# Performance work log

Hardware: AMD Instinct MI355X
Metric: run time of the kernel (lower is better)

## Reference

```python
import jax, jax.numpy as jnp
import numpy as np
import math

D = 2048
H = 8
DK = D // H // 2  # 128
NL = 3
EPS = 1e-6
SCALE = 1.0 / math.sqrt(DK)


def _ln(x, g, b):
    m = jnp.mean(x, axis=-1, keepdims=True)
    v = jnp.mean(jnp.square(x - m), axis=-1, keepdims=True)
    return (x - m) * jax.lax.rsqrt(v + EPS) * g + b


def _attn_layer(x, g, b, Wq, Wk, Wv):
    bs = x.shape[0]
    xn = _ln(x, g, b)
    # torch Linear: y = x @ W.T ; reshape to (bs, h, 2, d_k)
    q = (xn @ Wq.T).reshape(bs, H, 2, DK)
    k = (xn @ Wk.T).reshape(bs, H, 2, DK)
    v = (xn @ Wv.T).reshape(bs, H, 2, DK)
    s = jnp.einsum('bhpd,bhqd->bhpq', q, k) * SCALE  # tiny 2x2 scores
    a = jax.nn.softmax(s, axis=-1)
    o = jnp.einsum('bhpq,bhqd->bhpd', a, v).reshape(bs, D)
    return o + x


def _ff_layer(x, lnd_g, lnd_b, lnt_g, lnt_b, Wd1, bd1, Wd2, bd2, Wt1, bt1, Wt2, bt2):
    d, t = x[:, :D // 2], x[:, D // 2:]
    dn = _ln(d, lnd_g, lnd_b)
    tn = _ln(t, lnt_g, lnt_b)
    do = jax.nn.relu(dn @ Wd1.T + bd1) @ Wd2.T + bd2
    to = jax.nn.relu(tn @ Wt1.T + bt1) @ Wt2.T + bt2
    return jnp.concatenate([do, to], axis=-1) + x


def setup_inputs() -> dict:
    key = jax.random.key(0)
    ks = iter(jax.random.split(key, 64))
    s = 0.02
    inp = {}
    inp['x'] = jax.random.normal(next(ks), (8192, D), dtype=jnp.float32)
    # attention stacks: NL layers
    inp['attn_ln_g'] = jnp.ones((NL, D), jnp.float32)
    inp['attn_ln_b'] = jnp.zeros((NL, D), jnp.float32)
    inp['Wq'] = jax.random.normal(next(ks), (NL, D, D), jnp.float32) * s
    inp['Wk'] = jax.random.normal(next(ks), (NL, D, D), jnp.float32) * s
    inp['Wv'] = jax.random.normal(next(ks), (NL, D, D), jnp.float32) * s
    # feedforward stacks: NL-1 layers
    F = NL - 1
    hd = D // 2
    inp['ff_lnd_g'] = jnp.ones((F, hd), jnp.float32)
    inp['ff_lnd_b'] = jnp.zeros((F, hd), jnp.float32)
    inp['ff_lnt_g'] = jnp.ones((F, hd), jnp.float32)
    inp['ff_lnt_b'] = jnp.zeros((F, hd), jnp.float32)
    inp['Wd1'] = jax.random.normal(next(ks), (F, D, hd), jnp.float32) * s
    inp['bd1'] = jnp.zeros((F, D), jnp.float32)
    inp['Wd2'] = jax.random.normal(next(ks), (F, hd, D), jnp.float32) * s
    inp['bd2'] = jnp.zeros((F, hd), jnp.float32)
    inp['Wt1'] = jax.random.normal(next(ks), (F, D, hd), jnp.float32) * s
    inp['bt1'] = jnp.zeros((F, D), jnp.float32)
    inp['Wt2'] = jax.random.normal(next(ks), (F, hd, D), jnp.float32) * s
    inp['bt2'] = jnp.zeros((F, hd), jnp.float32)
    # output head
    inp['Wo1'] = jax.random.normal(next(ks), (hd, D), jnp.float32) * s
    inp['bo1'] = jnp.zeros((hd,), jnp.float32)
    inp['Wo2'] = jax.random.normal(next(ks), (1, hd), jnp.float32) * s
    inp['bo2'] = jnp.zeros((1,), jnp.float32)
    return inp


def reference(x, attn_ln_g, attn_ln_b, Wq, Wk, Wv,
              ff_lnd_g, ff_lnd_b, ff_lnt_g, ff_lnt_b,
              Wd1, bd1, Wd2, bd2, Wt1, bt1, Wt2, bt2,
              Wo1, bo1, Wo2, bo2):
    for n in range(NL - 1):
        x = _attn_layer(x, attn_ln_g[n], attn_ln_b[n], Wq[n], Wk[n], Wv[n])
        x = _ff_layer(x, ff_lnd_g[n], ff_lnd_b[n], ff_lnt_g[n], ff_lnt_b[n],
                      Wd1[n], bd1[n], Wd2[n], bd2[n], Wt1[n], bt1[n], Wt2[n], bt2[n])
    x = _attn_layer(x, attn_ln_g[-1], attn_ln_b[-1], Wq[-1], Wk[-1], Wv[-1])
    h = jax.nn.relu(x @ Wo1.T + bo1)
    return h @ Wo2.T + bo2  # [bs, 1]
```

## Files before the change

### kernel.cpp

```cpp
#include <hip/hip_runtime.h>
#include <stdint.h>


typedef __bf16 bf16x8 __attribute__((ext_vector_type(8)));
typedef float f32x4 __attribute__((ext_vector_type(4)));

static __device__ __forceinline__ float bf2f(unsigned short u) {
  unsigned int x = ((unsigned int)u) << 16;
  float f;
  __builtin_memcpy(&f, &x, 4);
  return f;
}
static __device__ __forceinline__ unsigned short f2bf(float f) {
  unsigned int x;
  __builtin_memcpy(&x, &f, 4);
  x += 0x7fffu + ((x >> 16) & 1u);
  return (unsigned short)(x >> 16);
}

static __device__ __forceinline__ void gload_lds16(const void* g, void* l) {
  __builtin_amdgcn_global_load_lds(
      (const __attribute__((address_space(1))) unsigned int*)g,
      (__attribute__((address_space(3))) unsigned int*)l, 16, 0, 0);
}

__global__ __launch_bounds__(256) void cvt_kernel(
    const float* __restrict__ in, unsigned short* __restrict__ out, long n) {
  const long i = ((long)blockIdx.x * 256 + threadIdx.x) * 4;
  if (i + 3 < n) {
    float4 f = *(const float4*)(in + i);
    *(ushort4*)(out + i) = make_ushort4(f2bf(f.x), f2bf(f.y), f2bf(f.z), f2bf(f.w));
  }
}

#define MAXSEG 14
struct CvtArgs {
  const float* src[MAXSEG];
  unsigned short* dst[MAXSEG];
  long pfx[MAXSEG + 1];
  int ns;
};
__global__ __launch_bounds__(256) void cvt_multi_kernel(CvtArgs a) {
  const long i = ((long)blockIdx.x * 256 + threadIdx.x) * 4;
  int s = 0;
  while (s + 1 < a.ns && i >= a.pfx[s + 1]) ++s;
  const long off = i - a.pfx[s];
  float4 f = *(const float4*)(a.src[s] + off);
  *(ushort4*)(a.dst[s] + off) =
      make_ushort4(f2bf(f.x), f2bf(f.y), f2bf(f.z), f2bf(f.w));
}

#define BARRIER __builtin_amdgcn_s_barrier()
#define LGKM(N)                                                     \
  do {                                                              \
    asm volatile("s_waitcnt lgkmcnt(" #N ")" ::: "memory");         \
    __builtin_amdgcn_sched_barrier(0);                              \
  } while (0)
#define VMC(N)                                                      \
  do {                                                              \
    asm volatile("s_waitcnt vmcnt(" #N ")" ::: "memory");           \
    __builtin_amdgcn_sched_barrier(0);                              \
  } while (0)

__global__ __launch_bounds__(512, 2) void gemm8_kernel(
    const unsigned short* __restrict__ A, int lda,
    const unsigned short* __restrict__ B, int K,
    void* __restrict__ Cp, int ldc, const float* __restrict__ bias,
    int relu, int out_f32, int resadd,
    const unsigned short* __restrict__ A2, const unsigned short* __restrict__ B2,
    void* __restrict__ C2p, const float* __restrict__ bias2, int dual) {
  extern __shared__ __align__(16) char smem[];

  const int tid = threadIdx.x;
  const int lane = tid & 63;
  const int w = tid >> 6;
  const int wm = w >> 2;
  const int wn = w & 3;

  const int gx = (int)gridDim.x;
  const int nwg = gx * (int)gridDim.y;
  const int orig = (int)blockIdx.y * gx + (int)blockIdx.x;
  const int qch = nwg >> 3, rch = nwg & 7, xcd = orig & 7, io = orig >> 3;
  const int wgid =
      (xcd < rch ? xcd * (qch + 1) : rch * (qch + 1) + (xcd - rch) * qch) + io;
  const int bx = wgid % gx;
  const int by = wgid / gx;
  const long brow = (long)by * 256;

  const unsigned short* Ap = A;
  const unsigned short* Bp = B;
  const float* bi = bias;
  void* Cq = Cp;
  long bcol;
  if (dual && bx >= (gx >> 1)) {
    Ap = A2; Bp = B2; bi = bias2; Cq = C2p;
    bcol = (long)(bx - (gx >> 1)) * 256;
  } else {
    bcol = (long)bx * 256;
  }

  const int NT = K >> 6;

  const int lrA = tid >> 3;
  const int scb = ((tid & 7) * 16) ^ (((tid >> 3) & 7) << 4);
  const unsigned wb = (unsigned)(tid & ~63) * 16;
  const long ldab = (long)lda * 2;
  const long ldbb = (long)K * 2;
  const char* gA = (const char*)Ap + (brow + lrA) * ldab + scb;
  const char* gB = (const char*)Bp + (bcol + lrA) * ldbb + scb;
  const long a64 = 64 * ldab, a128 = 128 * ldab, a192 = 192 * ldab;
  const long b64 = 64 * ldbb, b128 = 128 * ldbb, b192 = 192 * ldbb;

#define STAGE_A(bb, off)                                        \
  do {                                                          \
    gload_lds16(gA + (off), smem + (bb) + wb);                  \
    gload_lds16(gA + a64 + (off), smem + (bb) + 8192 + wb);     \
    gload_lds16(gA + a128 + (off), smem + (bb) + 16384 + wb);   \
    gload_lds16(gA + a192 + (off), smem + (bb) + 24576 + wb);   \
  } while (0)
#define STAGE_B(bb, off)                                        \
  do {                                                          \
    gload_lds16(gB + (off), smem + (bb) + 32768 + wb);          \
    gload_lds16(gB + b64 + (off), smem + (bb) + 40960 + wb);    \
    gload_lds16(gB + b128 + (off), smem + (bb) + 49152 + wb);   \
    gload_lds16(gB + b192 + (off), smem + (bb) + 57344 + wb);   \
  } while (0)

  f32x4 acc[8][4];
  const f32x4 fz = {0.f, 0.f, 0.f, 0.f};
#pragma unroll
  for (int m = 0; m < 8; ++m)
#pragma unroll
    for (int n = 0; n < 4; ++n) acc[m][n] = fz;

  const int frow = lane & 15;
  const int fkb = (lane >> 4) * 16;
  const int fswz = (lane & 7) << 4;

#define RDA(dst, CB, M, KK)                                                   \
  dst = *(const bf16x8*)(smem + (CB) + (wm * 128 + (M) * 16 + frow) * 128 +   \
                         (((KK) * 64 + fkb) ^ fswz))
#define RDB(dst, CB, N, KK)                                                   \
  dst = *(const bf16x8*)(smem + (CB) + 32768 +                                \
                         (wn * 64 + (N) * 16 + frow) * 128 +                  \
                         (((KK) * 64 + fkb) ^ fswz))

#define MM8(AF, MA, BF, NA, MO, NO)                                           \
  do {                                                                        \
    _Pragma("unroll") for (int kk = 0; kk < 2; ++kk)                          \
    _Pragma("unroll") for (int mm = 0; mm < 2; ++mm)                          \
    _Pragma("unroll") for (int nn = 0; nn < 2; ++nn)                          \
        acc[(MO) + mm][(NO) + nn] = __builtin_amdgcn_mfma_f32_16x16x32_bf16(  \
            AF[(MA) + mm][kk], BF[(NA) + nn][kk], acc[(MO) + mm][(NO) + nn],  \
            0, 0, 0);                                                         \
  } while (0)
#define MM8N(AF, BF, NB, NO)                                                  \
  do {                                                                        \
    _Pragma("unroll") for (int kk = 0; kk < 2; ++kk)                          \
    _Pragma("unroll") for (int mm = 0; mm < 4; ++mm)                          \
        acc[mm][(NO)] = __builtin_amdgcn_mfma_f32_16x16x32_bf16(              \
            AF[mm][kk], BF[(NB)][kk], acc[mm][(NO)], 0, 0, 0);                \
  } while (0)

  bf16x8 afL[4][2], afH[4][2], bfvL[2][2], bfvH[2][2];

  STAGE_A(0, 0);
  STAGE_B(0, 0);
  STAGE_A(65536, 128);
  STAGE_B(65536, 128);
  VMC(8);
  BARRIER;
  long soff = 256;

#define TILE_IT(T, CB)                                                        \
  do {                                                                        \
                            \
    RDB(bfvL[0][0], CB, 0, 0); RDB(bfvL[0][1], CB, 0, 1);                     \
    RDB(bfvL[1][0], CB, 1, 0); RDB(bfvL[1][1], CB, 1, 1);                     \
    RDA(afL[0][0], CB, 0, 0); RDA(afL[0][1], CB, 0, 1);                       \
    RDA(afL[1][0], CB, 1, 0); RDA(afL[1][1], CB, 1, 1);                       \
    RDA(afL[2][0], CB, 2, 0); RDA(afL[2][1], CB, 2, 1);                       \
    RDA(afL[3][0], CB, 3, 0); RDA(afL[3][1], CB, 3, 1);                       \
    LGKM(8);                    \
    BARRIER;                                                                  \
    LGKM(0);                                                                  \
    __builtin_amdgcn_s_setprio(1);                                            \
    MM8(afL, 0, bfvL, 0, 0, 0);                                               \
    MM8(afL, 2, bfvL, 0, 2, 0);                                               \
    __builtin_amdgcn_s_setprio(0);                                            \
    BARRIER;                                                                  \
                                              \
    RDB(bfvH[0][0], CB, 2, 0); RDB(bfvH[0][1], CB, 2, 1);                     \
    RDB(bfvH[1][0], CB, 3, 0); RDB(bfvH[1][1], CB, 3, 1);                     \
    BARRIER;                                                                  \
    LGKM(0);                                                                  \
    __builtin_amdgcn_s_setprio(1);                                            \
    MM8N(afL, bfvH, 0, 2);                                                    \
    MM8N(afL, bfvH, 1, 3);                                                    \
    __builtin_amdgcn_s_setprio(0);                                            \
    BARRIER;                                                                  \
                 \
                                \
    RDA(afH[0][0], CB, 4, 0); RDA(afH[0][1], CB, 4, 1);                       \
    RDA(afH[1][0], CB, 5, 0); RDA(afH[1][1], CB, 5, 1);                       \
    RDA(afH[2][0], CB, 6, 0); RDA(afH[2][1], CB, 6, 1);                       \
    RDA(afH[3][0], CB, 7, 0); RDA(afH[3][1], CB, 7, 1);                       \
    if ((T) + 2 < NT) STAGE_B(CB, soff);                                      \
    BARRIER;                                                                  \
    LGKM(0);                                                                  \
    __builtin_amdgcn_s_setprio(1);                                            \
    MM8(afH, 0, bfvL, 0, 4, 0);                                               \
    MM8(afH, 2, bfvL, 0, 6, 0);                                               \
    __builtin_amdgcn_s_setprio(0);                                            \
    BARRIER;                                                                  \
                 \
                                \
    if ((T) + 2 < NT) {                                                       \
      STAGE_A(CB, soff);                                                      \
      VMC(8);                                      \
    } else {                                                                  \
      VMC(0);                                                 \
    }                                                                         \
    BARRIER;                                                                  \
    __builtin_amdgcn_s_setprio(1);                                            \
    MM8(afH, 0, bfvH, 0, 4, 2);                                               \
    MM8(afH, 2, bfvH, 0, 6, 2);                                               \
    __builtin_amdgcn_s_setprio(0);                                            \
    BARRIER;                                                                  \
    soff += 128;                                                              \
  } while (0)

  for (int t = 0; t < NT; t += 2) {
    TILE_IT(t, 0);
    TILE_IT(t + 1, 65536);
  }

  const long rb0 = brow + wm * 128 + (lane >> 4) * 4;
  const long cb0 = bcol + wn * 64 + (lane & 15);
#pragma unroll
  for (int m = 0; m < 8; ++m) {
#pragma unroll
    for (int n = 0; n < 4; ++n) {
      const long col = cb0 + n * 16;
      const float bv = bi ? bi[col] : 0.f;
#pragma unroll
      for (int j = 0; j < 4; ++j) {
        const long r = rb0 + m * 16 + j;
        float v = acc[m][n][j] + bv;
        if (relu) v = fmaxf(v, 0.f);
        if (out_f32) {
          float* cp = (float*)Cq + r * (long)ldc + col;
          if (resadd) v += *cp;
          *cp = v;
        } else {
          ((unsigned short*)Cq)[r * (long)ldc + col] = f2bf(v);
        }
      }
    }
  }
#undef TILE_IT
#undef STAGE_A
#undef STAGE_B
#undef RDA
#undef RDB
#undef MM8
#undef MM8N
}

__global__ __launch_bounds__(256) void gemm_bt_kernel(
    const unsigned short* __restrict__ A, int lda,
    const unsigned short* __restrict__ B, int K,
    void* __restrict__ Cp, int ldc,
    const float* __restrict__ bias,
    const void* __restrict__ res, int res_mode, int ldres,
    int relu, int out_f32) {
  __shared__ __align__(16) unsigned short As[128 * 32];
  __shared__ __align__(16) unsigned short Bs[128 * 32];

  const int t = threadIdx.x;
  const int lane = t & 63;
  const int w = t >> 6;
  const int wr = (w >> 1) * 64;
  const int wc = (w & 1) * 64;
  const long brow = (long)blockIdx.y * 128;
  const long bcol = (long)blockIdx.x * 128;

  const int srow = lane >> 2;
  const int scol = (lane & 3) * 8;
  const unsigned short* Ab = A + (brow + w * 32 + srow) * (long)lda + scol;
  const unsigned short* Bb = B + (bcol + w * 32 + srow) * (long)K + scol;
  unsigned short* Asb = &As[(w * 32) * 32];
  unsigned short* Bsb = &Bs[(w * 32) * 32];

  f32x4 acc[4][4];
  const f32x4 fzero = {0.f, 0.f, 0.f, 0.f};
#pragma unroll
  for (int m = 0; m < 4; ++m)
#pragma unroll
    for (int n = 0; n < 4; ++n) acc[m][n] = fzero;

  const int fr = lane & 15;
  const int fk = (lane >> 4) * 8;

  for (int kt = 0; kt < K; kt += 32) {
    gload_lds16(Ab + kt, Asb);
    gload_lds16(Ab + 16 * (long)lda + kt, Asb + 16 * 32);
    gload_lds16(Bb + kt, Bsb);
    gload_lds16(Bb + 16 * (long)K + kt, Bsb + 16 * 32);
    __syncthreads();

    bf16x8 af[4], bfv[4];
#pragma unroll
    for (int m = 0; m < 4; ++m)
      af[m] = *(const bf16x8*)&As[(wr + m * 16 + fr) * 32 + fk];
#pragma unroll
    for (int n = 0; n < 4; ++n)
      bfv[n] = *(const bf16x8*)&Bs[(wc + n * 16 + fr) * 32 + fk];
#pragma unroll
    for (int m = 0; m < 4; ++m)
#pragma unroll
      for (int n = 0; n < 4; ++n)
        acc[m][n] = __builtin_amdgcn_mfma_f32_16x16x32_bf16(af[m], bfv[n],
                                                            acc[m][n], 0, 0, 0);
    __syncthreads();
  }

  const long rbase = brow + wr + (lane >> 4) * 4;
#pragma unroll
  for (int m = 0; m < 4; ++m) {
#pragma unroll
    for (int n = 0; n < 4; ++n) {
      const long col = bcol + wc + n * 16 + fr;
      const float bv = bias ? bias[col] : 0.f;
#pragma unroll
      for (int j = 0; j < 4; ++j) {
        const long r = rbase + m * 16 + j;
        float v = acc[m][n][j] + bv;
        if (relu) v = fmaxf(v, 0.f);
        if (res_mode == 1)
          v += ((const float*)res)[r * (long)ldres + col];
        else if (res_mode == 2)
          v += bf2f(((const unsigned short*)res)[r * (long)ldres + col]);
        if (out_f32)
          ((float*)Cp)[r * (long)ldc + col] = v;
        else
          ((unsigned short*)Cp)[r * (long)ldc + col] = f2bf(v);
      }
    }
  }
}

template <int L>
__global__ __launch_bounds__(256) void ln_kernel(
    const void* __restrict__ inp, int in_bf16, int ldin,
    const float* __restrict__ g, const float* __restrict__ b,
    unsigned short* __restrict__ outp, int ldout) {
  constexpr int VEC = L / 256;
  const long row = blockIdx.x;
  const int t = threadIdx.x;
  float v[VEC];
  if (in_bf16) {
    const unsigned short* p = (const unsigned short*)inp + row * (long)ldin + t * VEC;
#pragma unroll
    for (int i = 0; i < VEC; i += 4) {
      ushort4 u = *(const ushort4*)(p + i);
      v[i] = bf2f(u.x); v[i + 1] = bf2f(u.y); v[i + 2] = bf2f(u.z); v[i + 3] = bf2f(u.w);
    }
  } else {
    const float* p = (const float*)inp + row * (long)ldin + t * VEC;
#pragma unroll
    for (int i = 0; i < VEC; i += 4) {
      float4 f = *(const float4*)(p + i);
      v[i] = f.x; v[i + 1] = f.y; v[i + 2] = f.z; v[i + 3] = f.w;
    }
  }
  float s = 0.f, sq = 0.f;
#pragma unroll
  for (int i = 0; i < VEC; ++i) { s += v[i]; sq += v[i] * v[i]; }
#pragma unroll
  for (int off = 32; off; off >>= 1) {
    s += __shfl_xor(s, off, 64);
    sq += __shfl_xor(sq, off, 64);
  }
  __shared__ float red[8];
  if ((t & 63) == 0) { red[t >> 6] = s; red[4 + (t >> 6)] = sq; }
  __syncthreads();
  s = red[0] + red[1] + red[2] + red[3];
  sq = red[4] + red[5] + red[6] + red[7];
  const float mean = s * (1.f / L);
  const float var = sq * (1.f / L) - mean * mean;
  const float rstd = rsqrtf(var + 1e-6f);
  unsigned short* op = outp + row * (long)ldout + t * VEC;
  const float* gp = g + t * VEC;
  const float* bp = b + t * VEC;
#pragma unroll
  for (int i = 0; i < VEC; i += 4) {
    float4 gg = *(const float4*)(gp + i);
    float4 bb = *(const float4*)(bp + i);
    *(ushort4*)(op + i) = make_ushort4(
        f2bf((v[i + 0] - mean) * rstd * gg.x + bb.x),
        f2bf((v[i + 1] - mean) * rstd * gg.y + bb.y),
        f2bf((v[i + 2] - mean) * rstd * gg.z + bb.z),
        f2bf((v[i + 3] - mean) * rstd * gg.w + bb.w));
  }
}

__global__ __launch_bounds__(512) void attn_glue_kernel(
    const unsigned short* __restrict__ Q, const unsigned short* __restrict__ Kq,
    const unsigned short* __restrict__ V, int ld, const void* __restrict__ Xres,
    int res_bf16, void* __restrict__ Xout, int out_bf16,
    unsigned short* __restrict__ Xout_bf,
    unsigned short* __restrict__ DNp, unsigned short* __restrict__ TNp,
    const float* __restrict__ lnd_g, const float* __restrict__ lnd_b,
    const float* __restrict__ lnt_g, const float* __restrict__ lnt_b) {
  const long row = blockIdx.x;
  const int h = threadIdx.x >> 6;
  const int lane = threadIdx.x & 63;
  const long qbase = row * (long)ld + h * 256;
  const long xbase = row * 2048 + h * 256;
  const int d = lane * 2;

  ushort2 q0 = *(const ushort2*)&Q[qbase + d];
  ushort2 q1 = *(const ushort2*)&Q[qbase + 128 + d];
  ushort2 k0 = *(const ushort2*)&Kq[qbase + d];
  ushort2 k1 = *(const ushort2*)&Kq[qbase + 128 + d];
  ushort2 v0 = *(const ushort2*)&V[qbase + d];
  ushort2 v1 = *(const ushort2*)&V[qbase + 128 + d];

  const float q0x = bf2f(q0.x), q0y = bf2f(q0.y);
  const float q1x = bf2f(q1.x), q1y = bf2f(q1.y);
  const float k0x = bf2f(k0.x), k0y = bf2f(k0.y);
  const float k1x = bf2f(k1.x), k1y = bf2f(k1.y);

  float s00 = q0x * k0x + q0y * k0y;
  float s01 = q0x * k1x + q0y * k1y;
  float s10 = q1x * k0x + q1y * k0y;
  float s11 = q1x * k1x + q1y * k1y;
#pragma unroll
  for (int off = 32; off; off >>= 1) {
    s00 += __shfl_xor(s00, off, 64);
    s01 += __shfl_xor(s01, off, 64);
    s10 += __shfl_xor(s10, off, 64);
    s11 += __shfl_xor(s11, off, 64);
  }
  const float SC = 0.088388347648318447f;
  s00 *= SC; s01 *= SC; s10 *= SC; s11 *= SC;
  const float m0 = fmaxf(s00, s01), m1 = fmaxf(s10, s11);
  const float e00 = __expf(s00 - m0), e01 = __expf(s01 - m0);
  const float e10 = __expf(s10 - m1), e11 = __expf(s11 - m1);
  const float i0 = 1.f / (e00 + e01), i1 = 1.f / (e10 + e11);
  const float a00 = e00 * i0, a01 = e01 * i0;
  const float a10 = e10 * i1, a11 = e11 * i1;

  const float v0x = bf2f(v0.x), v0y = bf2f(v0.y);
  const float v1x = bf2f(v1.x), v1y = bf2f(v1.y);
  float o0x = a00 * v0x + a01 * v1x, o0y = a00 * v0y + a01 * v1y;
  float o1x = a10 * v0x + a11 * v1x, o1y = a10 * v0y + a11 * v1y;

  if (res_bf16) {
    const unsigned short* xr = (const unsigned short*)Xres + xbase;
    ushort2 ra = *(const ushort2*)&xr[d];
    ushort2 rb = *(const ushort2*)&xr[128 + d];
    o0x += bf2f(ra.x); o0y += bf2f(ra.y); o1x += bf2f(rb.x); o1y += bf2f(rb.y);
  } else {
    const float* xr = (const float*)Xres + xbase;
    float2 ra = *(const float2*)&xr[d];
    float2 rb = *(const float2*)&xr[128 + d];
    o0x += ra.x; o0y += ra.y; o1x += rb.x; o1y += rb.y;
  }
  if (Xout) {
    if (out_bf16) {
      unsigned short* xo = (unsigned short*)Xout + xbase;
      *(ushort2*)&xo[d] = make_ushort2(f2bf(o0x), f2bf(o0y));
      *(ushort2*)&xo[128 + d] = make_ushort2(f2bf(o1x), f2bf(o1y));
    } else {
      float* xo = (float*)Xout + xbase;
      *(float2*)&xo[d] = make_float2(o0x, o0y);
      *(float2*)&xo[128 + d] = make_float2(o1x, o1y);
    }
  }
  if (Xout_bf) {
    unsigned short* xb = Xout_bf + xbase;
    *(ushort2*)&xb[d] = make_ushort2(f2bf(o0x), f2bf(o0y));
    *(ushort2*)&xb[128 + d] = make_ushort2(f2bf(o1x), f2bf(o1y));
  }

  if (DNp) {
    float s4 = o0x + o0y + o1x + o1y;
    float q4 = o0x * o0x + o0y * o0y + o1x * o1x + o1y * o1y;
#pragma unroll
    for (int off = 32; off; off >>= 1) {
      s4 += __shfl_xor(s4, off, 64);
      q4 += __shfl_xor(q4, off, 64);
    }
    __shared__ float redS[8], redQ[8];
    if (lane == 0) { redS[h] = s4; redQ[h] = q4; }
    __syncthreads();
    const int b4 = (h >> 2) * 4;
    const float S = redS[b4] + redS[b4 + 1] + redS[b4 + 2] + redS[b4 + 3];
    const float Qs = redQ[b4] + redQ[b4 + 1] + redQ[b4 + 2] + redQ[b4 + 3];
    const float mean = S * (1.f / 1024.f);
    const float var = Qs * (1.f / 1024.f) - mean * mean;
    const float rstd = rsqrtf(var + 1e-6f);
    const float* gp = (h < 4) ? lnd_g : lnt_g;
    const float* bp = (h < 4) ? lnd_b : lnt_b;
    unsigned short* dst = ((h < 4) ? DNp : TNp) + row * 1024;
    const int hc = (h & 3) * 256 + d;
    float2 g0 = *(const float2*)&gp[hc];
    float2 b0 = *(const float2*)&bp[hc];
    *(ushort2*)&dst[hc] = make_ushort2(f2bf((o0x - mean) * rstd * g0.x + b0.x),
                                       f2bf((o0y - mean) * rstd * g0.y + b0.y));
    float2 g1 = *(const float2*)&gp[hc + 128];
    float2 b1 = *(const float2*)&bp[hc + 128];
    *(ushort2*)&dst[hc + 128] =
        make_ushort2(f2bf((o1x - mean) * rstd * g1.x + b1.x),
                     f2bf((o1y - mean) * rstd * g1.y + b1.y));
  }
}

__global__ __launch_bounds__(256) void final_matvec_kernel(
    const unsigned short* __restrict__ Hm, const float* __restrict__ wv,
    const float* __restrict__ b2, float* __restrict__ outp) {
  const long row = blockIdx.x;
  const int t = threadIdx.x;
  ushort4 hv = *(const ushort4*)&Hm[row * 1024 + t * 4];
  float4 wq = *(const float4*)&wv[t * 4];
  float s = bf2f(hv.x) * wq.x + bf2f(hv.y) * wq.y +
            bf2f(hv.z) * wq.z + bf2f(hv.w) * wq.w;
#pragma unroll
  for (int off = 32; off; off >>= 1) s += __shfl_xor(s, off, 64);
  __shared__ float red[4];
  if ((t & 63) == 0) red[t >> 6] = s;
  __syncthreads();
  if (t == 0) outp[row] = red[0] + red[1] + red[2] + red[3] + b2[0];
}

extern "C" void kernel_launch(void* const* d_in, const int* in_sizes, int n_in,
                              void* d_out, int out_size, void* d_ws,
                              size_t ws_size, hipStream_t stream) {
  const float* x_in = (const float*)d_in[0];
  const float* aln_g = (const float*)d_in[1];
  const float* aln_b = (const float*)d_in[2];
  const float* Wq_f = (const float*)d_in[3];
  const float* Wk_f = (const float*)d_in[4];
  const float* Wv_f = (const float*)d_in[5];
  const float* lnd_g = (const float*)d_in[6];
  const float* lnd_b = (const float*)d_in[7];
  const float* lnt_g = (const float*)d_in[8];
  const float* lnt_b = (const float*)d_in[9];
  const float* Wd1_f = (const float*)d_in[10];
  const float* bd1 = (const float*)d_in[11];
  const float* Wd2_f = (const float*)d_in[12];
  const float* bd2 = (const float*)d_in[13];
  const float* Wt1_f = (const float*)d_in[14];
  const float* bt1 = (const float*)d_in[15];
  const float* Wt2_f = (const float*)d_in[16];
  const float* bt2 = (const float*)d_in[17];
  const float* Wo1_f = (const float*)d_in[18];
  const float* bo1 = (const float*)d_in[19];
  const float* Wo2_f = (const float*)d_in[20];
  const float* bo2 = (const float*)d_in[21];

  const size_t R = 8192, D = 2048, HD = 1024;
  const size_t DD = D * D;
  const size_t WALL = (3 * 3 * DD + 4 * 2 * D * HD + HD * D) * 2;
  const size_t SLOT = 3 * DD * 2;
  const size_t ACT = R * D * 4 + R * D * 2 + R * 6144 * 2;

  auto cvt = [&](const float* src, unsigned short* dst, long n) {
    cvt_kernel<<<dim3((unsigned)(n / 1024)), dim3(256), 0, stream>>>(src, dst, n);
  };

  if (ws_size >= ACT + SLOT) {
    const bool planAll = ws_size >= ACT + WALL;
    hipFuncSetAttribute(reinterpret_cast<const void*>(gemm8_kernel),
                        hipFuncAttributeMaxDynamicSharedMemorySize, 131072);

    char* p = (char*)d_ws;
    float* Xf = (float*)p; p += R * D * 4;
    unsigned short* XN = (unsigned short*)p; p += R * D * 2;
    unsigned short* QKVb = (unsigned short*)p; p += R * 6144 * 2;
    unsigned short* Warea = (unsigned short*)p;

    unsigned short* H1d = QKVb;
    unsigned short* H1t = QKVb + R * 2048;
    unsigned short* Hfin = QKVb + R * 4096;
    unsigned short* DN = XN;
    unsigned short* TN = XN + R * HD;

    unsigned short* Wqkv_b = Warea;
    unsigned short* Wd1_b = Wqkv_b + 9 * DD;
    unsigned short* Wt1_b = Wd1_b + 2 * D * HD;
    unsigned short* Wd2_b = Wt1_b + 2 * D * HD;
    unsigned short* Wt2_b = Wd2_b + 2 * D * HD;
    unsigned short* Wo1_b = Wt2_b + 2 * D * HD;
    if (planAll) {
      CvtArgs ca;
      int s = 0;
      long pfx = 0;
      auto add = [&](const float* src, unsigned short* dst, long n) {
        ca.src[s] = src; ca.dst[s] = dst; ca.pfx[s] = pfx; pfx += n; ++s;
      };
      for (int n = 0; n < 3; ++n) {
        add(Wq_f + n * DD, Wqkv_b + n * 3 * DD + 0 * DD, (long)DD);
        add(Wk_f + n * DD, Wqkv_b + n * 3 * DD + 1 * DD, (long)DD);
        add(Wv_f + n * DD, Wqkv_b + n * 3 * DD + 2 * DD, (long)DD);
      }
      add(Wd1_f, Wd1_b, (long)(2 * D * HD));
      add(Wt1_f, Wt1_b, (long)(2 * D * HD));
      add(Wd2_f, Wd2_b, (long)(2 * D * HD));
      add(Wt2_f, Wt2_b, (long)(2 * D * HD));
      add(Wo1_f, Wo1_b, (long)(HD * D));
      ca.pfx[s] = pfx;
      ca.ns = s;
      cvt_multi_kernel<<<dim3((unsigned)(pfx / 1024)), dim3(256), 0, stream>>>(ca);
    }

    auto gemm8 = [&](const unsigned short* A, int lda, const unsigned short* B,
                     int N, int K, void* C, int ldc, const float* bias,
                     int relu, int of32, int resadd, const unsigned short* A2,
                     const unsigned short* B2, void* C2, const float* bias2) {
      const int dual = (A2 != nullptr);
      dim3 grid((dual ? 2 : 1) * (N / 256), 32);
      gemm8_kernel<<<grid, dim3(512), 131072, stream>>>(
          A, lda, B, K, C, ldc, bias, relu, of32, resadd, A2, B2, C2, bias2,
          dual);
    };

    for (int n = 0; n < 3; ++n) {
      ln_kernel<2048><<<8192, 256, 0, stream>>>(
          (n == 0) ? (const void*)x_in : (const void*)Xf, 0, 2048,
          aln_g + n * D, aln_b + n * D, XN, 2048);
      const unsigned short* Wqkv;
      if (planAll) {
        Wqkv = Wqkv_b + (size_t)n * 3 * DD;
      } else {
        cvt(Wq_f + n * DD, Warea + 0 * DD, DD);
        cvt(Wk_f + n * DD, Warea + 1 * DD, DD);
        cvt(Wv_f + n * DD, Warea + 2 * DD, DD);
        Wqkv = Warea;
      }
      gemm8(XN, 2048, Wqkv, 6144, 2048, QKVb, 6144, nullptr, 0, 0, 0,
            nullptr, nullptr, nullptr, nullptr);
      attn_glue_kernel<<<8192, 512, 0, stream>>>(
          QKVb, QKVb + 2048, QKVb + 4096, 6144,
          (n == 0) ? (const void*)x_in : (const void*)Xf, 0,
          (n < 2) ? (void*)Xf : nullptr, 0,
          (n == 2) ? XN : nullptr,
          (n < 2) ? DN : nullptr, (n < 2) ? TN : nullptr,
          (n < 2) ? lnd_g + n * HD : nullptr, (n < 2) ? lnd_b + n * HD : nullptr,
          (n < 2) ? lnt_g + n * HD : nullptr, (n < 2) ? lnt_b + n * HD : nullptr);

      if (n < 2) {
        const size_t fo = (size_t)n * D * HD;
        const unsigned short *w1d, *w1t, *w2d, *w2t;
        if (planAll) {
          w1d = Wd1_b + fo; w1t = Wt1_b + fo; w2d = Wd2_b + fo; w2t = Wt2_b + fo;
        } else {
          cvt(Wd1_f + fo, Warea + 0 * D * HD, D * HD);
          cvt(Wt1_f + fo, Warea + 1 * D * HD, D * HD);
          cvt(Wd2_f + fo, Warea + 2 * D * HD, D * HD);
          cvt(Wt2_f + fo, Warea + 3 * D * HD, D * HD);
          w1d = Warea; w1t = Warea + D * HD; w2d = Warea + 2 * D * HD;
          w2t = Warea + 3 * D * HD;
        }
        gemm8(DN, 1024, w1d, 2048, 1024, H1d, 2048, bd1 + n * D, 1, 0, 0,
              TN, w1t, H1t, bt1 + n * D);
        gemm8(H1d, 2048, w2d, 1024, 2048, Xf, 2048, bd2 + n * HD, 0, 1, 1,
              H1t, w2t, Xf + HD, bt2 + n * HD);
      }
    }

    const unsigned short* Wo1p;
    if (planAll) {
      Wo1p = Wo1_b;
    } else {
      cvt(Wo1_f, Warea, HD * D);
      Wo1p = Warea;
    }
    gemm8(XN, 2048, Wo1p, 1024, 2048, Hfin, 1024, bo1, 1, 0, 0,
          nullptr, nullptr, nullptr, nullptr);
    final_matvec_kernel<<<8192, 256, 0, stream>>>(Hfin, Wo2_f, bo2,
                                                  (float*)d_out);
    return;
  }

  const size_t PLB = R * D * 2;
  const size_t XFZ = R * D * 4;
  const size_t SLOT1 = DD * 2;
  const bool planAll = ws_size >= XFZ + 4 * PLB + WALL;
  const bool xIsF32 = planAll || ws_size >= XFZ + 4 * PLB + SLOT1;

  char* p = (char*)d_ws;
  float* Xf = nullptr;
  unsigned short* Xb = nullptr;
  if (xIsF32) { Xf = (float*)p; p += XFZ; } else { Xb = (unsigned short*)p; p += PLB; }
  unsigned short* XN = (unsigned short*)p; p += PLB;
  unsigned short* Qb = (unsigned short*)p; p += PLB;
  unsigned short* Kb = (unsigned short*)p; p += PLB;
  unsigned short* Vb = (unsigned short*)p; p += PLB;
  unsigned short* Warea = (unsigned short*)p;

  void* X = xIsF32 ? (void*)Xf : (void*)Xb;
  const int xres_mode = xIsF32 ? 1 : 2;
  unsigned short* H1 = Qb;
  unsigned short* DN = XN;
  unsigned short* TN = XN + R * HD;
  unsigned short* Hfin = Vb;

  unsigned short* Wq_b = Warea;
  unsigned short* Wk_b = Wq_b + 3 * DD;
  unsigned short* Wv_b = Wk_b + 3 * DD;
  unsigned short* Wd1_b = Wv_b + 3 * DD;
  unsigned short* Wd2_b = Wd1_b + 2 * D * HD;
  unsigned short* Wt1_b = Wd2_b + 2 * D * HD;
  unsigned short* Wt2_b = Wt1_b + 2 * D * HD;
  unsigned short* Wo1_b = Wt2_b + 2 * D * HD;
  if (planAll) {
    cvt(Wq_f, Wq_b, 3 * DD);
    cvt(Wk_f, Wk_b, 3 * DD);
    cvt(Wv_f, Wv_b, 3 * DD);
    cvt(Wd1_f, Wd1_b, 2 * D * HD);
    cvt(Wd2_f, Wd2_b, 2 * D * HD);
    cvt(Wt1_f, Wt1_b, 2 * D * HD);
    cvt(Wt2_f, Wt2_b, 2 * D * HD);
    cvt(Wo1_f, Wo1_b, HD * D);
  }
  auto wbf = [&](const float* src_base, unsigned short* pre_base, size_t off,
                 size_t cnt) -> const unsigned short* {
    if (planAll) return pre_base + off;
    cvt(src_base + off, Warea, (long)cnt);
    return Warea;
  };
  auto gemm = [&](const unsigned short* A, int lda, const unsigned short* B,
                  int N, int K, void* C, int ldc, const float* bias,
                  const void* res, int res_mode, int ldres, int relu, int of32) {
    dim3 grid(N / 128, 8192 / 128);
    gemm_bt_kernel<<<grid, dim3(256), 0, stream>>>(
        A, lda, B, K, C, ldc, bias, res, res_mode, ldres, relu, of32);
  };

  for (int n = 0; n < 3; ++n) {
    const void* lin = (n == 0) ? (const void*)x_in : (const void*)X;
    const int lin_bf16 = (n == 0) ? 0 : (xIsF32 ? 0 : 1);
    ln_kernel<2048><<<8192, 256, 0, stream>>>(lin, lin_bf16, 2048,
                                              aln_g + n * D, aln_b + n * D, XN, 2048);
    const size_t wo = (size_t)n * DD;
    gemm(XN, 2048, wbf(Wq_f, Wq_b, wo, DD), 2048, 2048, Qb, 2048,
         nullptr, nullptr, 0, 0, 0, 0);
    gemm(XN, 2048, wbf(Wk_f, Wk_b, wo, DD), 2048, 2048, Kb, 2048,
         nullptr, nullptr, 0, 0, 0, 0);
    gemm(XN, 2048, wbf(Wv_f, Wv_b, wo, DD), 2048, 2048, Vb, 2048,
         nullptr, nullptr, 0, 0, 0, 0);
    attn_glue_kernel<<<8192, 512, 0, stream>>>(
        Qb, Kb, Vb, 2048, (n == 0) ? (const void*)x_in : (const void*)X,
        (n == 0) ? 0 : (xIsF32 ? 0 : 1), X, xIsF32 ? 0 : 1,
        (n == 2 && xIsF32) ? XN : nullptr,
        nullptr, nullptr, nullptr, nullptr, nullptr, nullptr);

    if (n < 2) {
      const size_t fo = (size_t)n * D * HD;
      ln_kernel<1024><<<8192, 256, 0, stream>>>(X, !xIsF32, 2048,
                                                lnd_g + n * HD, lnd_b + n * HD, DN, 1024);
      const void* Xt = xIsF32 ? (const void*)(Xf + HD) : (const void*)(Xb + HD);
      ln_kernel<1024><<<8192, 256, 0, stream>>>(Xt, !xIsF32, 2048,
                                                lnt_g + n * HD, lnt_b + n * HD, TN, 1024);
      void* Xd2 = X;
      void* Xt2 = xIsF32 ? (void*)(Xf + HD) : (void*)(Xb + HD);
      gemm(DN, 1024, wbf(Wd1_f, Wd1_b, fo, D * HD), 2048, 1024, H1, 2048,
           bd1 + n * D, nullptr, 0, 0, 1, 0);
      gemm(H1, 2048, wbf(Wd2_f, Wd2_b, fo, D * HD), 1024, 2048, Xd2, 2048,
           bd2 + n * HD, Xd2, xres_mode, 2048, 0, xIsF32 ? 1 : 0);
      gemm(TN, 1024, wbf(Wt1_f, Wt1_b, fo, D * HD), 2048, 1024, H1, 2048,
           bt1 + n * D, nullptr, 0, 0, 1, 0);
      gemm(H1, 2048, wbf(Wt2_f, Wt2_b, fo, D * HD), 1024, 2048, Xt2, 2048,
           bt2 + n * HD, Xt2, xres_mode, 2048, 0, xIsF32 ? 1 : 0);
    }
  }

  const unsigned short* Afin = xIsF32 ? XN : Xb;
  gemm(Afin, 2048, wbf(Wo1_f, Wo1_b, 0, HD * D), 1024, 2048, Hfin, 1024,
       bo1, nullptr, 0, 0, 1, 0);
  final_matvec_kernel<<<8192, 256, 0, stream>>>(Hfin, Wo2_f, bo2, (float*)d_out);
}
```

Baseline: 1.322 ms.

## Replace 256x256 double-buffered GEMM with 256x128 single-buffered high-occupancy kernel

```diff
diff --git a/kernel.cpp b/kernel.cpp
--- a/kernel.cpp
+++ b/kernel.cpp
@@ -62,74 +62,62 @@
     __builtin_amdgcn_sched_barrier(0);                              \
   } while (0)
 
-__global__ __launch_bounds__(512, 2) void gemm8_kernel(
+__global__ __launch_bounds__(512, 4) void gemm2b_kernel(
     const unsigned short* __restrict__ A, int lda,
     const unsigned short* __restrict__ B, int K,
     void* __restrict__ Cp, int ldc, const float* __restrict__ bias,
     int relu, int out_f32, int resadd,
     const unsigned short* __restrict__ A2, const unsigned short* __restrict__ B2,
     void* __restrict__ C2p, const float* __restrict__ bias2, int dual) {
-  extern __shared__ __align__(16) char smem[];
+  __shared__ __align__(16) char smem[49152];
 
   const int tid = threadIdx.x;
   const int lane = tid & 63;
   const int w = tid >> 6;
-  const int wm = w >> 2;
-  const int wn = w & 3;
-
-  const int gx = (int)gridDim.x;
-  const int nwg = gx * (int)gridDim.y;
-  const int orig = (int)blockIdx.y * gx + (int)blockIdx.x;
-  const int qch = nwg >> 3, rch = nwg & 7, xcd = orig & 7, io = orig >> 3;
-  const int wgid =
-      (xcd < rch ? xcd * (qch + 1) : rch * (qch + 1) + (xcd - rch) * qch) + io;
-  const int bx = wgid % gx;
-  const int by = wgid / gx;
-  const long brow = (long)by * 256;
+  const int wm = w >> 1;
+  const int wn = w & 1;
+  const long brow = (long)blockIdx.y * 256;
 
   const unsigned short* Ap = A;
   const unsigned short* Bp = B;
   const float* bi = bias;
   void* Cq = Cp;
   long bcol;
+  const int gx = (int)gridDim.x;
+  const int bx = (int)blockIdx.x;
   if (dual && bx >= (gx >> 1)) {
     Ap = A2; Bp = B2; bi = bias2; Cq = C2p;
-    bcol = (long)(bx - (gx >> 1)) * 256;
+    bcol = (long)(bx - (gx >> 1)) * 128;
   } else {
-    bcol = (long)bx * 256;
+    bcol = (long)bx * 128;
   }
 
   const int NT = K >> 6;
 
   const int lrA = tid >> 3;
   const int scb = ((tid & 7) * 16) ^ (((tid >> 3) & 7) << 4);
-  const unsigned wb = (unsigned)(tid & ~63) * 16;
+  const unsigned wb = (unsigned)tid * 16;
   const long ldab = (long)lda * 2;
   const long ldbb = (long)K * 2;
   const char* gA = (const char*)Ap + (brow + lrA) * ldab + scb;
   const char* gB = (const char*)Bp + (bcol + lrA) * ldbb + scb;
   const long a64 = 64 * ldab, a128 = 128 * ldab, a192 = 192 * ldab;
-  const long b64 = 64 * ldbb, b128 = 128 * ldbb, b192 = 192 * ldbb;
-
-#define STAGE_A(bb, off)                                        \
+  const long b64 = 64 * ldbb;
+
+#define STAGE(off)                                              \
   do {                                                          \
-    gload_lds16(gA + (off), smem + (bb) + wb);                  \
-    gload_lds16(gA + a64 + (off), smem + (bb) + 8192 + wb);     \
-    gload_lds16(gA + a128 + (off), smem + (bb) + 16384 + wb);   \
-    gload_lds16(gA + a192 + (off), smem + (bb) + 24576 + wb);   \
+    gload_lds16(gA + (off), smem + (wb & ~1023u));              \
+    gload_lds16(gA + a64 + (off), smem + 8192 + (wb & ~1023u)); \
+    gload_lds16(gA + a128 + (off), smem + 16384 + (wb & ~1023u)); \
+    gload_lds16(gA + a192 + (off), smem + 24576 + (wb & ~1023u)); \
+    gload_lds16(gB + (off), smem + 32768 + (wb & ~1023u));      \
+    gload_lds16(gB + b64 + (off), smem + 40960 + (wb & ~1023u)); \
   } while (0)
-#define STAGE_B(bb, off)                                        \
-  do {                                                          \
-    gload_lds16(gB + (off), smem + (bb) + 32768 + wb);          \
-    gload_lds16(gB + b64 + (off), smem + (bb) + 40960 + wb);    \
-    gload_lds16(gB + b128 + (off), smem + (bb) + 49152 + wb);   \
-    gload_lds16(gB + b192 + (off), smem + (bb) + 57344 + wb);   \
-  } while (0)
-
-  f32x4 acc[8][4];
+
+  f32x4 acc[4][4];
   const f32x4 fz = {0.f, 0.f, 0.f, 0.f};
 #pragma unroll
-  for (int m = 0; m < 8; ++m)
+  for (int m = 0; m < 4; ++m)
 #pragma unroll
     for (int n = 0; n < 4; ++n) acc[m][n] = fz;
 
@@ -137,108 +125,54 @@
   const int fkb = (lane >> 4) * 16;
   const int fswz = (lane & 7) << 4;
 
-#define RDA(dst, CB, M, KK)                                                   \
-  dst = *(const bf16x8*)(smem + (CB) + (wm * 128 + (M) * 16 + frow) * 128 +   \
+#define RDA(dst, M, KK)                                                       \
+  dst = *(const bf16x8*)(smem + (wm * 64 + (M) * 16 + frow) * 128 +           \
                          (((KK) * 64 + fkb) ^ fswz))
-#define RDB(dst, CB, N, KK)                                                   \
-  dst = *(const bf16x8*)(smem + (CB) + 32768 +                                \
-                         (wn * 64 + (N) * 16 + frow) * 128 +                  \
+#define RDB(dst, N, KK)                                                       \
+  dst = *(const bf16x8*)(smem + 32768 + (wn * 64 + (N) * 16 + frow) * 128 +   \
                          (((KK) * 64 + fkb) ^ fswz))
 
-#define MM8(AF, MA, BF, NA, MO, NO)                                           \
+#define MM16(A4, B4)                                                          \
   do {                                                                        \
-    _Pragma("unroll") for (int kk = 0; kk < 2; ++kk)                          \
-    _Pragma("unroll") for (int mm = 0; mm < 2; ++mm)                          \
-    _Pragma("unroll") for (int nn = 0; nn < 2; ++nn)                          \
-        acc[(MO) + mm][(NO) + nn] = __builtin_amdgcn_mfma_f32_16x16x32_bf16(  \
-            AF[(MA) + mm][kk], BF[(NA) + nn][kk], acc[(MO) + mm][(NO) + nn],  \
-            0, 0, 0);                                                         \
+    _Pragma("unroll") for (int mm = 0; mm < 4; ++mm)                          \
+    _Pragma("unroll") for (int nn = 0; nn < 4; ++nn)                          \
+        acc[mm][nn] = __builtin_amdgcn_mfma_f32_16x16x32_bf16(                \
+            A4[mm], B4[nn], acc[mm][nn], 0, 0, 0);                            \
   } while (0)
-#define MM8N(AF, BF, NB, NO)                                                  \
-  do {                                                                        \
-    _Pragma("unroll") for (int kk = 0; kk < 2; ++kk)                          \
-    _Pragma("unroll") for (int mm = 0; mm < 4; ++mm)                          \
-        acc[mm][(NO)] = __builtin_amdgcn_mfma_f32_16x16x32_bf16(              \
-            AF[mm][kk], BF[(NB)][kk], acc[mm][(NO)], 0, 0, 0);                \
-  } while (0)
-
-  bf16x8 afL[4][2], afH[4][2], bfvL[2][2], bfvH[2][2];
-
-  STAGE_A(0, 0);
-  STAGE_B(0, 0);
-  STAGE_A(65536, 128);
-  STAGE_B(65536, 128);
-  VMC(8);
-  BARRIER;
-  long soff = 256;
-
-#define TILE_IT(T, CB)                                                        \
-  do {                                                                        \
-                            \
-    RDB(bfvL[0][0], CB, 0, 0); RDB(bfvL[0][1], CB, 0, 1);                     \
-    RDB(bfvL[1][0], CB, 1, 0); RDB(bfvL[1][1], CB, 1, 1);                     \
-    RDA(afL[0][0], CB, 0, 0); RDA(afL[0][1], CB, 0, 1);                       \
-    RDA(afL[1][0], CB, 1, 0); RDA(afL[1][1], CB, 1, 1);                       \
-    RDA(afL[2][0], CB, 2, 0); RDA(afL[2][1], CB, 2, 1);                       \
-    RDA(afL[3][0], CB, 3, 0); RDA(afL[3][1], CB, 3, 1);                       \
-    LGKM(8);                    \
-    BARRIER;                                                                  \
-    LGKM(0);                                                                  \
-    __builtin_amdgcn_s_setprio(1);                                            \
-    MM8(afL, 0, bfvL, 0, 0, 0);                                               \
-    MM8(afL, 2, bfvL, 0, 2, 0);                                               \
-    __builtin_amdgcn_s_setprio(0);                                            \
-    BARRIER;                                                                  \
-                                              \
-    RDB(bfvH[0][0], CB, 2, 0); RDB(bfvH[0][1], CB, 2, 1);                     \
-    RDB(bfvH[1][0], CB, 3, 0); RDB(bfvH[1][1], CB, 3, 1);                     \
-    BARRIER;                                                                  \
-    LGKM(0);                                                                  \
-    __builtin_amdgcn_s_setprio(1);                                            \
-    MM8N(afL, bfvH, 0, 2);                                                    \
-    MM8N(afL, bfvH, 1, 3);                                                    \
-    __builtin_amdgcn_s_setprio(0);                                            \
-    BARRIER;                                                                  \
-                 \
-                                \
-    RDA(afH[0][0], CB, 4, 0); RDA(afH[0][1], CB, 4, 1);                       \
-    RDA(afH[1][0], CB, 5, 0); RDA(afH[1][1], CB, 5, 1);                       \
-    RDA(afH[2][0], CB, 6, 0); RDA(afH[2][1], CB, 6, 1);                       \
-    RDA(afH[3][0], CB, 7, 0); RDA(afH[3][1], CB, 7, 1);                       \
-    if ((T) + 2 < NT) STAGE_B(CB, soff);                                      \
-    BARRIER;                                                                  \
-    LGKM(0);                                                                  \
-    __builtin_amdgcn_s_setprio(1);                                            \
-    MM8(afH, 0, bfvL, 0, 4, 0);                                               \
-    MM8(afH, 2, bfvL, 0, 6, 0);                                               \
-    __builtin_amdgcn_s_setprio(0);                                            \
-    BARRIER;                                                                  \
-                 \
-                                \
-    if ((T) + 2 < NT) {                                                       \
-      STAGE_A(CB, soff);                                                      \
-      VMC(8);                                      \
-    } else {                                                                  \
-      VMC(0);                                                 \
-    }                                                                         \
-    BARRIER;                                                                  \
-    __builtin_amdgcn_s_setprio(1);                                            \
-    MM8(afH, 0, bfvH, 0, 4, 2);                                               \
-    MM8(afH, 2, bfvH, 0, 6, 2);                                               \
-    __builtin_amdgcn_s_setprio(0);                                            \
-    BARRIER;                                                                  \
-    soff += 128;                                                              \
-  } while (0)
-
-  for (int t = 0; t < NT; t += 2) {
-    TILE_IT(t, 0);
-    TILE_IT(t + 1, 65536);
-  }
-
-  const long rb0 = brow + wm * 128 + (lane >> 4) * 4;
+
+  STAGE(0);
+  long soff = 128;
+
+  for (int t = 0; t < NT; ++t) {
+    VMC(0);
+    BARRIER;
+
+    bf16x8 a0[4], b0[4];
+    RDA(a0[0], 0, 0); RDA(a0[1], 1, 0); RDA(a0[2], 2, 0); RDA(a0[3], 3, 0);
+    RDB(b0[0], 0, 0); RDB(b0[1], 1, 0); RDB(b0[2], 2, 0); RDB(b0[3], 3, 0);
+    LGKM(0);
+    __builtin_amdgcn_s_setprio(1);
+    MM16(a0, b0);
+    __builtin_amdgcn_s_setprio(0);
+    __builtin_amdgcn_sched_barrier(0);
+
+    bf16x8 a1[4], b1[4];
+    RDA(a1[0], 0, 1); RDA(a1[1], 1, 1); RDA(a1[2], 2, 1); RDA(a1[3], 3, 1);
+    RDB(b1[0], 0, 1); RDB(b1[1], 1, 1); RDB(b1[2], 2, 1); RDB(b1[3], 3, 1);
+    LGKM(0);
+    BARRIER;
+    if (t + 1 < NT) STAGE(soff);
+    __builtin_amdgcn_s_setprio(1);
+    MM16(a1, b1);
+    __builtin_amdgcn_s_setprio(0);
+    __builtin_amdgcn_sched_barrier(0);
+    soff += 128;
+  }
+
+  const long rb0 = brow + wm * 64 + (lane >> 4) * 4;
   const long cb0 = bcol + wn * 64 + (lane & 15);
 #pragma unroll
-  for (int m = 0; m < 8; ++m) {
+  for (int m = 0; m < 4; ++m) {
 #pragma unroll
     for (int n = 0; n < 4; ++n) {
       const long col = cb0 + n * 16;
@@ -258,13 +192,10 @@
       }
     }
   }
-#undef TILE_IT
-#undef STAGE_A
-#undef STAGE_B
+#undef STAGE
 #undef RDA
 #undef RDB
-#undef MM8
-#undef MM8N
+#undef MM16
 }
 
 __global__ __launch_bounds__(256) void gemm_bt_kernel(
@@ -573,8 +504,6 @@
 
   if (ws_size >= ACT + SLOT) {
     const bool planAll = ws_size >= ACT + WALL;
-    hipFuncSetAttribute(reinterpret_cast<const void*>(gemm8_kernel),
-                        hipFuncAttributeMaxDynamicSharedMemorySize, 131072);
 
     char* p = (char*)d_ws;
     float* Xf = (float*)p; p += R * D * 4;
@@ -616,13 +545,13 @@
       cvt_multi_kernel<<<dim3((unsigned)(pfx / 1024)), dim3(256), 0, stream>>>(ca);
     }
 
-    auto gemm8 = [&](const unsigned short* A, int lda, const unsigned short* B,
-                     int N, int K, void* C, int ldc, const float* bias,
-                     int relu, int of32, int resadd, const unsigned short* A2,
-                     const unsigned short* B2, void* C2, const float* bias2) {
+    auto gemm = [&](const unsigned short* A, int lda, const unsigned short* B,
+                    int N, int K, void* C, int ldc, const float* bias,
+                    int relu, int of32, int resadd, const unsigned short* A2,
+                    const unsigned short* B2, void* C2, const float* bias2) {
       const int dual = (A2 != nullptr);
-      dim3 grid((dual ? 2 : 1) * (N / 256), 32);
-      gemm8_kernel<<<grid, dim3(512), 131072, stream>>>(
+      dim3 grid((dual ? 2 : 1) * (N / 128), 32);
+      gemm2b_kernel<<<grid, dim3(512), 0, stream>>>(
           A, lda, B, K, C, ldc, bias, relu, of32, resadd, A2, B2, C2, bias2,
           dual);
     };
@@ -640,8 +569,8 @@
         cvt(Wv_f + n * DD, Warea + 2 * DD, DD);
         Wqkv = Warea;
       }
-      gemm8(XN, 2048, Wqkv, 6144, 2048, QKVb, 6144, nullptr, 0, 0, 0,
-            nullptr, nullptr, nullptr, nullptr);
+      gemm(XN, 2048, Wqkv, 6144, 2048, QKVb, 6144, nullptr, 0, 0, 0,
+           nullptr, nullptr, nullptr, nullptr);
       attn_glue_kernel<<<8192, 512, 0, stream>>>(
           QKVb, QKVb + 2048, QKVb + 4096, 6144,
           (n == 0) ? (const void*)x_in : (const void*)Xf, 0,
@@ -664,10 +593,10 @@
           w1d = Warea; w1t = Warea + D * HD; w2d = Warea + 2 * D * HD;
           w2t = Warea + 3 * D * HD;
         }
-        gemm8(DN, 1024, w1d, 2048, 1024, H1d, 2048, bd1 + n * D, 1, 0, 0,
-              TN, w1t, H1t, bt1 + n * D);
-        gemm8(H1d, 2048, w2d, 1024, 2048, Xf, 2048, bd2 + n * HD, 0, 1, 1,
-              H1t, w2t, Xf + HD, bt2 + n * HD);
+        gemm(DN, 1024, w1d, 2048, 1024, H1d, 2048, bd1 + n * D, 1, 0, 0,
+             TN, w1t, H1t, bt1 + n * D);
+        gemm(H1d, 2048, w2d, 1024, 2048, Xf, 2048, bd2 + n * HD, 0, 1, 1,
+             H1t, w2t, Xf + HD, bt2 + n * HD);
       }
     }
 
@@ -678,8 +607,8 @@
       cvt(Wo1_f, Warea, HD * D);
       Wo1p = Warea;
     }
-    gemm8(XN, 2048, Wo1p, 1024, 2048, Hfin, 1024, bo1, 1, 0, 0,
-          nullptr, nullptr, nullptr, nullptr);
+    gemm(XN, 2048, Wo1p, 1024, 2048, Hfin, 1024, bo1, 1, 0, 0,
+         nullptr, nullptr, nullptr, nullptr);
     final_matvec_kernel<<<8192, 256, 0, stream>>>(Hfin, Wo2_f, bo2,
                                                   (float*)d_out);
     return;
```

After: 1.250 ms. 1.06x faster.
